# Optimization experiments

Measured on AMD Instinct MI355X. Metric: run time of the kernel, lower is better.

The kernel has to match this reference:

```python
import jax, jax.numpy as jnp
import numpy as np

N = 100000
F_IN = 512
H1 = 256  # nhid*2
H2 = 128  # nhid
C = 4
E = 3200000


def setup_inputs() -> dict:
    key = jax.random.key(0)
    ks = jax.random.split(key, 8)
    x = jax.random.normal(ks[0], (N, F_IN), dtype=jnp.float32)
    edge_index = jax.random.randint(ks[1], (2, E), 0, N, dtype=jnp.int64)
    s = 1.0 / np.sqrt(F_IN)
    W1 = jax.random.uniform(ks[2], (F_IN, H1), jnp.float32, -s, s)
    b1 = jnp.zeros((H1,), jnp.float32)
    s2 = 1.0 / np.sqrt(H1)
    W2 = jax.random.uniform(ks[3], (H1, H2), jnp.float32, -s2, s2)
    b2 = jnp.zeros((H2,), jnp.float32)
    s3 = 1.0 / np.sqrt(H2)
    Wl = jax.random.uniform(ks[4], (H2, C), jnp.float32, -s3, s3)
    bl = jax.random.uniform(ks[5], (C,), jnp.float32, -s3, s3)
    return {"x": x, "edge_index": edge_index, "W1": W1, "b1": b1,
            "W2": W2, "b2": b2, "Wl": Wl, "bl": bl}


def gcn_conv(x, W, b, src, dst, n):
    # PyG GCNConv: add self loops, symmetric normalization D^-1/2 (A+I) D^-1/2
    h = x @ W  # [N, out]
    ones = jnp.ones((src.shape[0],), h.dtype)
    deg = jax.ops.segment_sum(ones, dst, num_segments=n) + 1.0  # +1 self loop
    dinv = jax.lax.rsqrt(deg)
    norm = dinv[src] * dinv[dst]  # [E]
    msg = h[src] * norm[:, None]  # gather + scale
    agg = jax.ops.segment_sum(msg, dst, num_segments=n)  # scatter-add
    agg = agg + h * (dinv * dinv)[:, None]  # self-loop contribution (norm=1/deg)
    return agg + b


def reference(x, edge_index, W1, b1, W2, b2, Wl, bl):
    src, dst = edge_index[0], edge_index[1]
    h = jax.nn.relu(gcn_conv(x, W1, b1, src, dst, N))
    h = jax.nn.relu(gcn_conv(h, W2, b2, src, dst, N))
    logits = h @ Wl + bl
    return jax.nn.log_softmax(logits, axis=-1)
```

## Files before the change

kernel.cpp:

```cpp
#include <hip/hip_runtime.h>
#include <hip/hip_bf16.h>
#include <cstdint>
#include <cstddef>

__device__ __forceinline__ float bf2f(unsigned short u) {
    return __uint_as_float(((unsigned int)u) << 16);
}
__device__ __forceinline__ unsigned short f2bf(float f) {
    unsigned int u = __float_as_uint(f);
    unsigned int r = (u + 0x7fff + ((u >> 16) & 1)) >> 16;
    return (unsigned short)r;
}

using bf16x8 = __attribute__((ext_vector_type(8))) short;
using f32x4  = __attribute__((ext_vector_type(4))) float;
typedef float f32x2 __attribute__((ext_vector_type(2)));

#define FP8_SCALE    64.0f
#define FP8_INVSCALE 0.015625f

__device__ __forceinline__ unsigned char f2fp8(float v) {
    int p = __builtin_amdgcn_cvt_pk_fp8_f32(v, v, 0, false);
    return (unsigned char)(p & 0xFF);
}
__device__ __forceinline__ void acc_fp8x8(unsigned lo, unsigned hi, float* a) {
    f32x2 f0 = __builtin_amdgcn_cvt_pk_f32_fp8((int)lo, false);
    f32x2 f1 = __builtin_amdgcn_cvt_pk_f32_fp8((int)lo, true);
    f32x2 f2 = __builtin_amdgcn_cvt_pk_f32_fp8((int)hi, false);
    f32x2 f3 = __builtin_amdgcn_cvt_pk_f32_fp8((int)hi, true);
    a[0] += f0[0]; a[1] += f0[1]; a[2] += f1[0]; a[3] += f1[1];
    a[4] += f2[0]; a[5] += f2[1]; a[6] += f3[0]; a[7] += f3[1];
}

__device__ __forceinline__ bf16x8 cvt8(float4 a, float4 b) {
    union { unsigned u[4]; bf16x8 v; } r;
    asm("v_cvt_pk_bf16_f32 %0, %1, %2" : "=v"(r.u[0]) : "v"(a.x), "v"(a.y));
    asm("v_cvt_pk_bf16_f32 %0, %1, %2" : "=v"(r.u[1]) : "v"(a.z), "v"(a.w));
    asm("v_cvt_pk_bf16_f32 %0, %1, %2" : "=v"(r.u[2]) : "v"(b.x), "v"(b.y));
    asm("v_cvt_pk_bf16_f32 %0, %1, %2" : "=v"(r.u[3]) : "v"(b.z), "v"(b.w));
    return r.v;
}

#define BKT_SHIFT 9
#define BKT_NODES 512
#define BKT_CAP   18432
#define BIN_TILE  4096
#define PAD_G     8
#define BKT_PADMAX (BKT_NODES * (PAD_G - 1))

__global__ __launch_bounds__(256) void bin_kernel(const int* __restrict__ eidx, int E,
                                                  int nb, int ntiles,
                                                  int* __restrict__ gcur,
                                                  unsigned* __restrict__ binned) {
    __shared__ int cnt[256];
    __shared__ int base[256];
    const int tid = threadIdx.x;
    for (int t = blockIdx.x; t < ntiles; t += gridDim.x) {
        cnt[tid] = 0;
        __syncthreads();
        int s[16], d[16];
        unsigned pk[16];
        #pragma unroll
        for (int j = 0; j < 16; ++j) {
            int e = t * BIN_TILE + j * 256 + tid;
            if (e < E) {
                s[j] = eidx[e];
                d[j] = eidx[E + e];
                int b = d[j] >> BKT_SHIFT;
                int r = atomicAdd(&cnt[b], 1);
                pk[j] = ((unsigned)b << 16) | (unsigned)r;
            } else {
                pk[j] = 0xFFFFFFFFu;
            }
        }
        __syncthreads();
        if (tid < nb) {
            int c = cnt[tid];
            base[tid] = c ? atomicAdd(&gcur[tid], c) : 0;
        }
        __syncthreads();
        #pragma unroll
        for (int j = 0; j < 16; ++j) {
            if (pk[j] != 0xFFFFFFFFu) {
                int b = (int)(pk[j] >> 16);
                int pos = base[b] + (int)(pk[j] & 0xFFFFu);
                if (pos < BKT_CAP)
                    binned[(size_t)b * BKT_CAP + pos] =
                        ((unsigned)s[j] << BKT_SHIFT) | ((unsigned)d[j] & (BKT_NODES - 1));
            }
        }
        __syncthreads();
    }
}

__global__ __launch_bounds__(256) void csr_build_kernel(const unsigned* __restrict__ binned,
                                                        const int* __restrict__ gcur,
                                                        int* __restrict__ rowptr,
                                                        int* __restrict__ deg,
                                                        float* __restrict__ dinv,
                                                        int* __restrict__ csr_src,
                                                        int nb, int n) {
    __shared__ int cnt[BKT_NODES];
    __shared__ int sbase[256];
    __shared__ int wsum[4];
    const int b = blockIdx.x;
    const int base_node = b << BKT_SHIFT;
    const int tid = threadIdx.x, lane = tid & 63, wave = tid >> 6;

    int c = (tid < nb) ? (min(gcur[tid], BKT_CAP) + BKT_PADMAX) : 0;
    int inc = c;
    #pragma unroll
    for (int off = 1; off < 64; off <<= 1) {
        int t = __shfl_up(inc, off, 64);
        if (lane >= off) inc += t;
    }
    if (lane == 63) wsum[wave] = inc;
    __syncthreads();
    int wbase = 0;
    #pragma unroll
    for (int w = 0; w < 4; ++w)
        if (w < wave) wbase += wsum[w];
    sbase[tid] = wbase + inc - c;
    __syncthreads();
    const int gb = sbase[b];
    __syncthreads();

    for (int i = tid; i < BKT_NODES; i += 256) cnt[i] = 0;
    __syncthreads();
    const int m = min(gcur[b], BKT_CAP);
    const unsigned* eb = binned + (size_t)b * BKT_CAP;
    for (int i = tid; i < m; i += 256)
        atomicAdd(&cnt[eb[i] & (BKT_NODES - 1)], 1);
    __syncthreads();

    int c0 = cnt[2 * tid], c1 = cnt[2 * tid + 1];
    int pc0 = (c0 + PAD_G - 1) & ~(PAD_G - 1);
    int pc1 = (c1 + PAD_G - 1) & ~(PAD_G - 1);
    int s = pc0 + pc1;
    int inc2 = s;
    #pragma unroll
    for (int off = 1; off < 64; off <<= 1) {
        int t = __shfl_up(inc2, off, 64);
        if (lane >= off) inc2 += t;
    }
    __syncthreads();
    if (lane == 63) wsum[wave] = inc2;
    __syncthreads();
    int wbase2 = 0;
    #pragma unroll
    for (int w = 0; w < 4; ++w)
        if (w < wave) wbase2 += wsum[w];
    int excl = wbase2 + inc2 - s;
    int node0 = base_node + 2 * tid;
    int st0 = gb + excl, st1 = gb + excl + pc0;
    if (node0 < n) {
        rowptr[node0] = st0;
        deg[node0] = pc0;
        dinv[node0] = rsqrtf((float)c0 + 1.0f);
        for (int q = c0; q < pc0; ++q) csr_src[st0 + q] = n;
    }
    if (node0 + 1 < n) {
        rowptr[node0 + 1] = st1;
        deg[node0 + 1] = pc1;
        dinv[node0 + 1] = rsqrtf((float)c1 + 1.0f);
        for (int q = c1; q < pc1; ++q) csr_src[st1 + q] = n;
    }
    __syncthreads();
    cnt[2 * tid] = st0;
    cnt[2 * tid + 1] = st1;
    __syncthreads();

    for (int i = tid; i < m; i += 256) {
        unsigned p = eb[i];
        int pos = atomicAdd(&cnt[p & (BKT_NODES - 1)], 1);
        csr_src[pos] = (int)(p >> BKT_SHIFT);
    }
}

__global__ __launch_bounds__(256) void hist_kernel(const int* __restrict__ dst, int E,
                                                   int* __restrict__ deg) {
    int i = blockIdx.x * blockDim.x + threadIdx.x;
    int stride = gridDim.x * blockDim.x;
    for (int e = i; e < E; e += stride) atomicAdd(&deg[dst[e]], 1);
}

__global__ __launch_bounds__(256) void fill_kernel(const int* __restrict__ eidx, int E,
                                                   int* __restrict__ cursor,
                                                   int* __restrict__ csr_src) {
    int e = blockIdx.x * blockDim.x + threadIdx.x;
    if (e < E) {
        int s = eidx[e];
        int d = eidx[E + e];
        int pos = atomicAdd(&cursor[d], 1);
        csr_src[pos] = s;
    }
}

__global__ __launch_bounds__(256) void scan_kernel(const int* __restrict__ deg,
                                                   int* __restrict__ rowptr, int n) {
    __shared__ int wsum[4];
    __shared__ int carry_s;
    int tid = threadIdx.x, lane = tid & 63, wave = tid >> 6;
    if (tid == 0) carry_s = 0;
    __syncthreads();
    const int CHUNK = 16;
    const int PER_ITER = 256 * CHUNK;
    for (int base = 0; base < n; base += PER_ITER) {
        int idx0 = base + tid * CHUNK;
        int v[CHUNK];
        int s = 0;
        #pragma unroll
        for (int j = 0; j < CHUNK; ++j) {
            int i = idx0 + j;
            v[j] = (i < n) ? deg[i] : 0;
            s += v[j];
        }
        int inc = s;
        #pragma unroll
        for (int off = 1; off < 64; off <<= 1) {
            int t = __shfl_up(inc, off, 64);
            if (lane >= off) inc += t;
        }
        if (lane == 63) wsum[wave] = inc;
        __syncthreads();
        int wbase = 0;
        #pragma unroll
        for (int w = 0; w < 4; ++w)
            if (w < wave) wbase += wsum[w];
        int total_iter = wsum[0] + wsum[1] + wsum[2] + wsum[3];
        int carry = carry_s;
        __syncthreads();
        if (tid == 0) carry_s = carry + total_iter;
        int run = carry + wbase + (inc - s);
        #pragma unroll
        for (int j = 0; j < CHUNK; ++j) {
            int i = idx0 + j;
            if (i < n) rowptr[i] = run;
            run += v[j];
        }
        __syncthreads();
    }
    if (tid == 0) rowptr[n] = carry_s;
}

__global__ __launch_bounds__(256) void dinv_kernel(const int* __restrict__ deg,
                                                   float* __restrict__ dinv, int n) {
    int i = blockIdx.x * blockDim.x + threadIdx.x;
    if (i < n) dinv[i] = rsqrtf((float)deg[i] + 1.0f);
}

__global__ __launch_bounds__(256) void wt_kernel(const float* __restrict__ W1,
                                                 const float* __restrict__ W2,
                                                 unsigned short* __restrict__ W1F,
                                                 unsigned short* __restrict__ W2F) {
    int i = blockIdx.x * 256 + threadIdx.x;
    const int n1 = 512 * 256;
    if (i < n1) {
        int blk = i >> 9, r = i & 511;
        int lane = r >> 3, jj = r & 7;
        int k0 = (blk >> 4) << 5;
        int f = blk & 15;
        int quad = lane >> 4, l16 = lane & 15;
        int k = k0 + quad * 8 + jj;
        int nn = f * 16 + l16;
        W1F[i] = f2bf(W1[(size_t)k * 256 + nn]);
    } else {
        int j = i - n1;
        if (j < 256 * 128) {
            int blk = j >> 9, r = j & 511;
            int lane = r >> 3, jj = r & 7;
            int k0 = (blk >> 3) << 5;
            int f = blk & 7;
            int quad = lane >> 4, l16 = lane & 15;
            int k = k0 + quad * 8 + jj;
            int nn = f * 16 + l16;
            W2F[j] = f2bf(W2[(size_t)k * 128 + nn]);
        }
    }
}

__global__ __launch_bounds__(256, 4) void gemm1_kernel(const float* __restrict__ x,
                                                       const unsigned short* __restrict__ W1F,
                                                       const float* __restrict__ dinv,
                                                       unsigned char* __restrict__ C,
                                                       int M) {
    __shared__ float As[2][4096];
    const int tid = threadIdx.x;
    const int wave = tid >> 6, lane = tid & 63;
    const int quad = lane >> 4, l16 = lane & 15;
    const int m0 = blockIdx.x * 64;

    const float* sbase[4];
    #pragma unroll
    for (int c = 0; c < 4; ++c) {
        int row  = (wave * 4 + c) * 4 + (lane >> 4);
        int grow = min(m0 + row, M - 1);
        int scb  = ((lane & 15) << 4) ^ ((row & 7) << 4);
        sbase[c] = x + (size_t)grow * 512 + (scb >> 2);
    }
    const int r   = wave * 16 + l16;
    const int swz = (r & 7) << 4;
    const int rb  = r * 256;

    #pragma unroll
    for (int c = 0; c < 4; ++c)
        __builtin_amdgcn_global_load_lds(sbase[c], &As[0][(wave * 4 + c) * 256], 16, 0, 0);
    __syncthreads();

    f32x4 acc[4][4] = {};
    for (int t = 0; t < 8; ++t) {
        const int cur = t & 1;
        if (t < 7) {
            #pragma unroll
            for (int c = 0; c < 4; ++c)
                __builtin_amdgcn_global_load_lds(sbase[c] + (t + 1) * 64,
                                                 &As[cur ^ 1][(wave * 4 + c) * 256], 16, 0, 0);
        }
        const char* ab = reinterpret_cast<const char*>(&As[cur][0]);
        #pragma unroll
        for (int ks = 0; ks < 2; ++ks) {
            int cb = (ks << 7) + (quad << 5);
            float4 a0 = *reinterpret_cast<const float4*>(ab + rb + (cb ^ swz));
            float4 a1 = *reinterpret_cast<const float4*>(ab + rb + ((cb + 16) ^ swz));
            bf16x8 af = cvt8(a0, a1);
            const unsigned short* wp = W1F + ((((t << 1) + ks) << 4) << 9) + lane * 8;
            #pragma unroll
            for (int i = 0; i < 4; ++i) {
                #pragma unroll
                for (int ct = 0; ct < 4; ++ct) {
                    bf16x8 bfr = *reinterpret_cast<const bf16x8*>(wp + (((i << 2) + ct) << 9));
                    acc[i][ct] = __builtin_amdgcn_mfma_f32_16x16x32_bf16(af, bfr, acc[i][ct], 0, 0, 0);
                }
            }
        }
        __syncthreads();
    }

    #pragma unroll
    for (int rr = 0; rr < 4; ++rr) {
        int row = m0 + wave * 16 + quad * 4 + rr;
        if (row < M) {
            float dv = dinv[row] * FP8_SCALE;
            #pragma unroll
            for (int i = 0; i < 4; ++i)
                #pragma unroll
                for (int ct = 0; ct < 4; ++ct)
                    C[(size_t)row * 256 + i * 64 + ct * 16 + l16] = f2fp8(acc[i][ct][rr] * dv);
        }
    }
}

__device__ __forceinline__ int a2_idx(int row, int col) {
    int byte = (row << 9) + (col << 1);
    byte ^= (row & 7) << 4;
    return byte >> 1;
}

__global__ __launch_bounds__(256, 5) void agg1_gemm2_kernel(const unsigned char* __restrict__ hs1,
                                                            const float* __restrict__ dinv,
                                                            const int* __restrict__ rowptr,
                                                            const int* __restrict__ deg,
                                                            const int* __restrict__ csr_src,
                                                            const float* __restrict__ b1,
                                                            const unsigned short* __restrict__ W2F,
                                                            unsigned short* __restrict__ hs2,
                                                            int n) {
    __shared__ __align__(16) short As2[64 * 256];
    const int tid = threadIdx.x;
    const int m0 = blockIdx.x * 64;

    {
        const int lane = tid & 31;
        const int sub = tid >> 5;
        const unsigned char* tab = hs1 + (size_t)lane * 8;
        float4 blo = *(reinterpret_cast<const float4*>(b1) + lane * 2);
        float4 bhi = *(reinterpret_cast<const float4*>(b1) + lane * 2 + 1);
        float bvals[8] = {blo.x, blo.y, blo.z, blo.w, bhi.x, bhi.y, bhi.z, bhi.w};
        for (int g = 0; g < 8; ++g) {
            int row = g * 8 + sub;
            int node = m0 + row;
            float h[8] = {};
            if (node < n) {
                float a[8] = {};
                uint2 v0 = *reinterpret_cast<const uint2*>(tab + (size_t)node * 256);
                acc_fp8x8(v0.x, v0.y, a);
                int e0 = rowptr[node], e1 = e0 + deg[node];
                int p = e0;
                for (; p + 8 <= e1; p += 8) {
                    int s[8];
                    #pragma unroll
                    for (int u = 0; u < 8; ++u) s[u] = csr_src[p + u];
                    uint2 w[8];
                    #pragma unroll
                    for (int u = 0; u < 8; ++u)
                        w[u] = *reinterpret_cast<const uint2*>(tab + (size_t)s[u] * 256);
                    #pragma unroll
                    for (int u = 0; u < 8; ++u)
                        acc_fp8x8(w[u].x, w[u].y, a);
                }
                for (; p < e1; ++p) {
                    int s = csr_src[p];
                    uint2 w = *reinterpret_cast<const uint2*>(tab + (size_t)s * 256);
                    acc_fp8x8(w.x, w.y, a);
                }
                float dv = dinv[node] * FP8_INVSCALE;
                #pragma unroll
                for (int j = 0; j < 8; ++j)
                    h[j] = fmaxf(fmaf(a[j], dv, bvals[j]), 0.f);
            }
            bf16x8 o;
            #pragma unroll
            for (int j = 0; j < 8; ++j) o[j] = (short)f2bf(h[j]);
            *reinterpret_cast<bf16x8*>(&As2[a2_idx(row, lane * 8)]) = o;
        }
    }
    __syncthreads();

    const int wave = tid >> 6, lane = tid & 63;
    const int quad = lane >> 4, l16 = lane & 15;
    const int arow = wave * 16 + l16;
    f32x4 acc[2][4] = {};
    #pragma unroll
    for (int k0 = 0; k0 < 256; k0 += 32) {
        bf16x8 af = *reinterpret_cast<const bf16x8*>(&As2[a2_idx(arow, k0 + quad * 8)]);
        #pragma unroll
        for (int i = 0; i < 2; ++i) {
            #pragma unroll
            for (int ct = 0; ct < 4; ++ct) {
                bf16x8 bfr = *reinterpret_cast<const bf16x8*>(
                    W2F + ((((k0 >> 5) << 3) + i * 4 + ct) << 9) + lane * 8);
                acc[i][ct] = __builtin_amdgcn_mfma_f32_16x16x32_bf16(af, bfr, acc[i][ct], 0, 0, 0);
            }
        }
    }
    #pragma unroll
    for (int r = 0; r < 4; ++r) {
        int row = m0 + wave * 16 + quad * 4 + r;
        if (row < n) {
            float dv = dinv[row];
            #pragma unroll
            for (int i = 0; i < 2; ++i)
                #pragma unroll
                for (int ct = 0; ct < 4; ++ct)
                    hs2[(size_t)row * 128 + i * 64 + ct * 16 + l16] = f2bf(acc[i][ct][r] * dv);
        }
    }
}

__global__ __launch_bounds__(256) void agg2_head_kernel(const unsigned short* __restrict__ hs,
                                                        const float* __restrict__ dinv,
                                                        const int* __restrict__ rowptr,
                                                        const int* __restrict__ deg,
                                                        const int* __restrict__ csr_src,
                                                        const float* __restrict__ bias,
                                                        const float* __restrict__ Wl,
                                                        const float* __restrict__ bl,
                                                        float* __restrict__ out, int n) {
    constexpr int LANES = 16, H = 128, NPB = 16;
    int sub = threadIdx.x / LANES;
    int lane = threadIdx.x % LANES;
    int node = blockIdx.x * NPB + sub;
    if (node >= n) return;
    const unsigned short* tab = hs + (size_t)lane * 8;
    float a[8];
    bf16x8 v0 = *reinterpret_cast<const bf16x8*>(tab + (size_t)node * H);
    #pragma unroll
    for (int j = 0; j < 8; ++j) a[j] = bf2f((unsigned short)v0[j]);
    int e0 = rowptr[node], e1 = e0 + deg[node];
    int p = e0;
    for (; p + 8 <= e1; p += 8) {
        int s[8];
        #pragma unroll
        for (int u = 0; u < 8; ++u) s[u] = csr_src[p + u];
        bf16x8 w[8];
        #pragma unroll
        for (int u = 0; u < 8; ++u)
            w[u] = *reinterpret_cast<const bf16x8*>(tab + (size_t)s[u] * H);
        #pragma unroll
        for (int u = 0; u < 8; ++u)
            #pragma unroll
            for (int j = 0; j < 8; ++j) a[j] += bf2f((unsigned short)w[u][j]);
    }
    for (; p < e1; ++p) {
        int s = csr_src[p];
        bf16x8 w = *reinterpret_cast<const bf16x8*>(tab + (size_t)s * H);
        #pragma unroll
        for (int j = 0; j < 8; ++j) a[j] += bf2f((unsigned short)w[j]);
    }
    float dv = dinv[node];
    float4 blo = *(reinterpret_cast<const float4*>(bias) + lane * 2);
    float4 bhi = *(reinterpret_cast<const float4*>(bias) + lane * 2 + 1);
    float bvals[8] = {blo.x, blo.y, blo.z, blo.w, bhi.x, bhi.y, bhi.z, bhi.w};
    float h[8];
    #pragma unroll
    for (int j = 0; j < 8; ++j)
        h[j] = fmaxf(fmaf(a[j], dv, bvals[j]), 0.f);
    float p0 = 0.f, p1 = 0.f, p2 = 0.f, p3 = 0.f;
    #pragma unroll
    for (int j = 0; j < 8; ++j) {
        float4 w = *reinterpret_cast<const float4*>(Wl + (size_t)(lane * 8 + j) * 4);
        p0 = fmaf(h[j], w.x, p0); p1 = fmaf(h[j], w.y, p1);
        p2 = fmaf(h[j], w.z, p2); p3 = fmaf(h[j], w.w, p3);
    }
    #pragma unroll
    for (int m = 1; m < 16; m <<= 1) {
        p0 += __shfl_xor(p0, m, 16);
        p1 += __shfl_xor(p1, m, 16);
        p2 += __shfl_xor(p2, m, 16);
        p3 += __shfl_xor(p3, m, 16);
    }
    if (lane == 0) {
        p0 += bl[0]; p1 += bl[1]; p2 += bl[2]; p3 += bl[3];
        float mx = fmaxf(fmaxf(p0, p1), fmaxf(p2, p3));
        float s = __expf(p0 - mx) + __expf(p1 - mx) + __expf(p2 - mx) + __expf(p3 - mx);
        float lse = mx + __logf(s);
        *(reinterpret_cast<float4*>(out) + node) = make_float4(p0 - lse, p1 - lse, p2 - lse, p3 - lse);
    }
}

extern "C" void kernel_launch(void* const* d_in, const int* in_sizes, int n_in,
                              void* d_out, int out_size, void* d_ws, size_t ws_size,
                              hipStream_t stream) {
    const float* x  = (const float*)d_in[0];
    const int* eidx = (const int*)d_in[1];
    const float* W1 = (const float*)d_in[2];
    const float* b1 = (const float*)d_in[3];
    const float* W2 = (const float*)d_in[4];
    const float* b2 = (const float*)d_in[5];
    const float* Wl = (const float*)d_in[6];
    const float* bl = (const float*)d_in[7];
    float* out = (float*)d_out;

    const int n = in_sizes[0] / 512;
    const int E = in_sizes[1] / 2;
    const int nb = (n + BKT_NODES - 1) >> BKT_SHIFT;

    char* ws = (char*)d_ws;
    size_t off = 0;
    auto alloc = [&](size_t bytes) -> void* {
        void* p = ws + off;
        off += (bytes + 255) & ~(size_t)255;
        return p;
    };
    unsigned char*  hA  = (unsigned char*)alloc((size_t)(n + 1) * 256);
    unsigned short* hB  = (unsigned short*)alloc((size_t)(n + 1) * 128 * 2);
    unsigned short* W1F = (unsigned short*)alloc((size_t)256 * 512 * 2);
    unsigned short* W2F = (unsigned short*)alloc((size_t)128 * 256 * 2);
    int* deg     = (int*)alloc((size_t)n * 4);
    int* rowptr  = (int*)alloc(((size_t)n + 1) * 4);
    int* cursor  = (int*)alloc((size_t)n * 4);
    float* dinv  = (float*)alloc((size_t)n * 4);
    int* csr_src = (int*)alloc(((size_t)E + (size_t)nb * BKT_PADMAX + 64) * 4);
    int* gcur    = (int*)alloc((size_t)nb * 4);
    size_t need_binned = off + (size_t)nb * BKT_CAP * 4 + 256;
    unsigned* binned = (unsigned*)alloc((size_t)nb * BKT_CAP * 4);

    if (need_binned <= ws_size && nb <= 256 && n < (1 << 23)) {
        hipMemsetAsync(gcur, 0, (size_t)nb * 4, stream);
        int ntiles = (E + BIN_TILE - 1) / BIN_TILE;
        bin_kernel<<<dim3(256), dim3(256), 0, stream>>>(eidx, E, nb, ntiles, gcur, binned);
        csr_build_kernel<<<dim3(nb), dim3(256), 0, stream>>>(binned, gcur, rowptr, deg, dinv,
                                                             csr_src, nb, n);
    } else {
        hipMemsetAsync(deg, 0, (size_t)n * 4, stream);
        hist_kernel<<<dim3(1024), dim3(256), 0, stream>>>(eidx + E, E, deg);
        scan_kernel<<<dim3(1), dim3(256), 0, stream>>>(deg, rowptr, n);
        dinv_kernel<<<dim3((n + 255) / 256), dim3(256), 0, stream>>>(deg, dinv, n);
        hipMemcpyAsync(cursor, rowptr, (size_t)n * 4, hipMemcpyDeviceToDevice, stream);
        fill_kernel<<<dim3((E + 255) / 256), dim3(256), 0, stream>>>(eidx, E, cursor, csr_src);
    }

    hipMemsetAsync(hA + (size_t)n * 256, 0, 256, stream);
    hipMemsetAsync(hB + (size_t)n * 128, 0, 128 * 2, stream);

    wt_kernel<<<dim3((512 * 256 + 256 * 128 + 255) / 256), dim3(256), 0, stream>>>(
        W1, W2, W1F, W2F);

    const int mblocks = (n + 63) / 64;

    gemm1_kernel<<<dim3(mblocks), dim3(256), 0, stream>>>(x, W1F, dinv, hA, n);

    agg1_gemm2_kernel<<<dim3(mblocks), dim3(256), 0, stream>>>(
        hA, dinv, rowptr, deg, csr_src, b1, W2F, hB, n);

    agg2_head_kernel<<<dim3((n + 15) / 16), dim3(256), 0, stream>>>(
        hB, dinv, rowptr, deg, csr_src, b2, Wl, bl, out, n);
}
```

Before: 694.3 us.

## Store layer-2 features as FP8 and restructure gemm1 wave tiling

The layer-2 hidden features hB are now stored as scaled FP8 instead of bf16, halving the bytes gathered per edge in the second aggregation kernel, which decodes them with the existing fp8 accumulate helper and unscales by the inverse factor. Separately, gemm1 now assigns each wave a 64-column slice across all 64 rows. Each wave loads its four W1 fragments once per k-step and reuses them across four A row tiles, instead of loading all sixteen fragments per row tile. The cost is lower precision in the second-layer messages and more LDS reads of A per wave.

After: 634.4 us. -8.6%, faster.

```diff
diff --git a/kernel.cpp b/kernel.cpp
--- a/kernel.cpp
+++ b/kernel.cpp
@@ -298,9 +298,7 @@
         int scb  = ((lane & 15) << 4) ^ ((row & 7) << 4);
         sbase[c] = x + (size_t)grow * 512 + (scb >> 2);
     }
-    const int r   = wave * 16 + l16;
-    const int swz = (r & 7) << 4;
-    const int rb  = r * 256;
+    const int swz = (l16 & 7) << 4;
 
     #pragma unroll
     for (int c = 0; c < 4; ++c)
@@ -319,33 +317,40 @@
         const char* ab = reinterpret_cast<const char*>(&As[cur][0]);
         #pragma unroll
         for (int ks = 0; ks < 2; ++ks) {
-            int cb = (ks << 7) + (quad << 5);
-            float4 a0 = *reinterpret_cast<const float4*>(ab + rb + (cb ^ swz));
-            float4 a1 = *reinterpret_cast<const float4*>(ab + rb + ((cb + 16) ^ swz));
-            bf16x8 af = cvt8(a0, a1);
-            const unsigned short* wp = W1F + ((((t << 1) + ks) << 4) << 9) + lane * 8;
+            const int cb = (ks << 7) + (quad << 5);
+            const unsigned short* wp =
+                W1F + (((((t << 1) + ks) << 4) + (wave << 2)) << 9) + lane * 8;
+            bf16x8 bfr0 = *reinterpret_cast<const bf16x8*>(wp);
+            bf16x8 bfr1 = *reinterpret_cast<const bf16x8*>(wp + 512);
+            bf16x8 bfr2 = *reinterpret_cast<const bf16x8*>(wp + 1024);
+            bf16x8 bfr3 = *reinterpret_cast<const bf16x8*>(wp + 1536);
             #pragma unroll
-            for (int i = 0; i < 4; ++i) {
+            for (int am = 0; am < 4; ++am) {
+                const char* rp = ab + ((am * 16 + l16) << 8);
+                float4 a0 = *reinterpret_cast<const float4*>(rp + (cb ^ swz));
+                float4 a1 = *reinterpret_cast<const float4*>(rp + ((cb + 16) ^ swz));
+                bf16x8 af = cvt8(a0, a1);
+                acc[am][0] = __builtin_amdgcn_mfma_f32_16x16x32_bf16(af, bfr0, acc[am][0], 0, 0, 0);
+                acc[am][1] = __builtin_amdgcn_mfma_f32_16x16x32_bf16(af, bfr1, acc[am][1], 0, 0, 0);
+                acc[am][2] = __builtin_amdgcn_mfma_f32_16x16x32_bf16(af, bfr2, acc[am][2], 0, 0, 0);
+                acc[am][3] = __builtin_amdgcn_mfma_f32_16x16x32_bf16(af, bfr3, acc[am][3], 0, 0, 0);
+            }
+        }
+        __syncthreads();
+    }
+
+    #pragma unroll
+    for (int am = 0; am < 4; ++am) {
+        #pragma unroll
+        for (int rr = 0; rr < 4; ++rr) {
+            int row = m0 + am * 16 + quad * 4 + rr;
+            if (row < M) {
+                float dv = dinv[row] * FP8_SCALE;
                 #pragma unroll
-                for (int ct = 0; ct < 4; ++ct) {
-                    bf16x8 bfr = *reinterpret_cast<const bf16x8*>(wp + (((i << 2) + ct) << 9));
-                    acc[i][ct] = __builtin_amdgcn_mfma_f32_16x16x32_bf16(af, bfr, acc[i][ct], 0, 0, 0);
-                }
+                for (int bn = 0; bn < 4; ++bn)
+                    C[(size_t)row * 256 + wave * 64 + bn * 16 + l16] =
+                        f2fp8(acc[am][bn][rr] * dv);
             }
-        }
-        __syncthreads();
-    }
-
-    #pragma unroll
-    for (int rr = 0; rr < 4; ++rr) {
-        int row = m0 + wave * 16 + quad * 4 + rr;
-        if (row < M) {
-            float dv = dinv[row] * FP8_SCALE;
-            #pragma unroll
-            for (int i = 0; i < 4; ++i)
-                #pragma unroll
-                for (int ct = 0; ct < 4; ++ct)
-                    C[(size_t)row * 256 + i * 64 + ct * 16 + l16] = f2fp8(acc[i][ct][rr] * dv);
         }
     }
 }
@@ -363,7 +368,7 @@
                                                             const int* __restrict__ csr_src,
                                                             const float* __restrict__ b1,
                                                             const unsigned short* __restrict__ W2F,
-                                                            unsigned short* __restrict__ hs2,
+                                                            unsigned char* __restrict__ hs2,
                                                             int n) {
     __shared__ __align__(16) short As2[64 * 256];
     const int tid = threadIdx.x;
@@ -437,17 +442,18 @@
     for (int r = 0; r < 4; ++r) {
         int row = m0 + wave * 16 + quad * 4 + r;
         if (row < n) {
-            float dv = dinv[row];
+            float dv = dinv[row] * FP8_SCALE;
             #pragma unroll
             for (int i = 0; i < 2; ++i)
                 #pragma unroll
                 for (int ct = 0; ct < 4; ++ct)
-                    hs2[(size_t)row * 128 + i * 64 + ct * 16 + l16] = f2bf(acc[i][ct][r] * dv);
-        }
-    }
-}
-
-__global__ __launch_bounds__(256) void agg2_head_kernel(const unsigned short* __restrict__ hs,
+                    hs2[(size_t)row * 128 + i * 64 + ct * 16 + l16] =
+                        f2fp8(acc[i][ct][r] * dv);
+        }
+    }
+}
+
+__global__ __launch_bounds__(256) void agg2_head_kernel(const unsigned char* __restrict__ hs,
                                                         const float* __restrict__ dinv,
                                                         const int* __restrict__ rowptr,
                                                         const int* __restrict__ deg,
@@ -461,33 +467,30 @@
     int lane = threadIdx.x % LANES;
     int node = blockIdx.x * NPB + sub;
     if (node >= n) return;
-    const unsigned short* tab = hs + (size_t)lane * 8;
-    float a[8];
-    bf16x8 v0 = *reinterpret_cast<const bf16x8*>(tab + (size_t)node * H);
-    #pragma unroll
-    for (int j = 0; j < 8; ++j) a[j] = bf2f((unsigned short)v0[j]);
+    const unsigned char* tab = hs + (size_t)lane * 8;
+    float a[8] = {};
+    uint2 v0 = *reinterpret_cast<const uint2*>(tab + (size_t)node * H);
+    acc_fp8x8(v0.x, v0.y, a);
     int e0 = rowptr[node], e1 = e0 + deg[node];
     int p = e0;
     for (; p + 8 <= e1; p += 8) {
         int s[8];
         #pragma unroll
         for (int u = 0; u < 8; ++u) s[u] = csr_src[p + u];
-        bf16x8 w[8];
+        uint2 w[8];
         #pragma unroll
         for (int u = 0; u < 8; ++u)
-            w[u] = *reinterpret_cast<const bf16x8*>(tab + (size_t)s[u] * H);
+            w[u] = *reinterpret_cast<const uint2*>(tab + (size_t)s[u] * H);
         #pragma unroll
         for (int u = 0; u < 8; ++u)
-            #pragma unroll
-            for (int j = 0; j < 8; ++j) a[j] += bf2f((unsigned short)w[u][j]);
+            acc_fp8x8(w[u].x, w[u].y, a);
     }
     for (; p < e1; ++p) {
         int s = csr_src[p];
-        bf16x8 w = *reinterpret_cast<const bf16x8*>(tab + (size_t)s * H);
-        #pragma unroll
-        for (int j = 0; j < 8; ++j) a[j] += bf2f((unsigned short)w[j]);
-    }
-    float dv = dinv[node];
+        uint2 w = *reinterpret_cast<const uint2*>(tab + (size_t)s * H);
+        acc_fp8x8(w.x, w.y, a);
+    }
+    float dv = dinv[node] * FP8_INVSCALE;
     float4 blo = *(reinterpret_cast<const float4*>(bias) + lane * 2);
     float4 bhi = *(reinterpret_cast<const float4*>(bias) + lane * 2 + 1);
     float bvals[8] = {blo.x, blo.y, blo.z, blo.w, bhi.x, bhi.y, bhi.z, bhi.w};
@@ -543,7 +546,7 @@
         return p;
     };
     unsigned char*  hA  = (unsigned char*)alloc((size_t)(n + 1) * 256);
-    unsigned short* hB  = (unsigned short*)alloc((size_t)(n + 1) * 128 * 2);
+    unsigned char*  hB  = (unsigned char*)alloc((size_t)(n + 1) * 128);
     unsigned short* W1F = (unsigned short*)alloc((size_t)256 * 512 * 2);
     unsigned short* W2F = (unsigned short*)alloc((size_t)128 * 256 * 2);
     int* deg     = (int*)alloc((size_t)n * 4);
@@ -571,7 +574,7 @@
     }
 
     hipMemsetAsync(hA + (size_t)n * 256, 0, 256, stream);
-    hipMemsetAsync(hB + (size_t)n * 128, 0, 128 * 2, stream);
+    hipMemsetAsync(hB + (size_t)n * 128, 0, 128, stream);
 
     wt_kernel<<<dim3((512 * 256 + 256 * 128 + 255) / 256), dim3(256), 0, stream>>>(
         W1, W2, W1F, W2F);
```
